# Kernel optimization log

Hardware: AMD Instinct MI355X
Metric: run time of the kernel (lower is better)

The kernel has to match this reference:

```python
import jax, jax.numpy as jnp
import numpy as np

TABLE_SIZE = 256
I16_MIN, I16_MAX = -32768.0, 32767.0
I8_MIN, I8_MAX = -128.0, 127.0
MAX_SOFTMAX_VALUE = 1.0
OUT_SCALE = MAX_SOFTMAX_VALUE * 2.0 / 255.0            # int8 output scale
EXP_OUT_SCALE = 2.0 / 65535.0                          # qint16 exp output scale
RECIP_OUT_SCALE = (1.0 / 0.1) * 2.0 / 65535.0          # qint16 reciprocal output scale
# (xmin, xmax, kind) in ascending x order; 'table' = 256-entry LUT, 'line' = linear fit
EXP_REGIONS = [(-40.0, -20.0, 'line'), (-20.0, -10.0, 'table'), (-10.0, 0.0, 'table'), (0.0, 1.0, 'line')]
RECIP_REGIONS = [(0.001, 0.1, 'line'), (0.1, 250.0, 'table'), (250.0, 500.0, 'table'), (500.0, 700.0, 'line')]


def _quant(y, out_scale, qmin, qmax):
    return jnp.clip(jnp.round(y / out_scale), qmin, qmax)


def _piecewise(x, func, regions, out_scale, qmin, qmax):
    """Piecewise quantized approximation of func: constant / line / 256-entry
    table regions, returning quantized (integer-valued float) outputs."""
    left_c = _quant(func(jnp.float32(regions[0][0])), out_scale, qmin, qmax)
    y = left_c * jnp.ones_like(x)
    for xmin, xmax, kind in regions:
        if kind == 'table':
            xs = jnp.linspace(xmin, xmax, TABLE_SIZE)
            tab = _quant(func(xs), out_scale, qmin, qmax)
            idx = jnp.clip(jnp.round((x - xmin) * ((TABLE_SIZE - 1) / (xmax - xmin))), 0, TABLE_SIZE - 1).astype(jnp.int32)
            y_r = tab[idx]
        else:
            y0 = func(jnp.float32(xmin))
            y1 = func(jnp.float32(xmax))
            y_r = _quant(y0 + (x - xmin) * ((y1 - y0) / (xmax - xmin)), out_scale, qmin, qmax)
        y = jnp.where(x >= xmin, y_r, y)
    right_c = _quant(func(jnp.float32(regions[-1][1])), out_scale, qmin, qmax)
    return jnp.where(x > regions[-1][1], right_c, y)


def setup_inputs() -> dict:
    key = jax.random.key(0)
    k1, _ = jax.random.split(key)
    data = jax.random.randint(k1, (32, 128, 80, 80), -128, 128, dtype=jnp.int32)  # int8 repr, zp=0
    data_scale = jnp.array([0.0625], dtype=jnp.float32)
    return {"data": data, "data_scale": data_scale}


def reference(data, data_scale):
    ds = data_scale[0]
    C = data.shape[1]
    shift = float(np.ceil(np.log2(C)))  # rescale_shift for the exp-sum
    # max-subtract in the integer domain, dequantize diff (zero_point = 0)
    qmax = jnp.max(data, axis=1, keepdims=True)
    xd = (data - qmax).astype(jnp.float32) * ds  # [B,C,H,W], in (-inf, 0]
    # quantized exp via piecewise tables -> qint16 with EXP_OUT_SCALE
    exp_q = _piecewise(xd, jnp.exp, EXP_REGIONS, EXP_OUT_SCALE, I16_MIN, I16_MAX)
    # sum over channels, right-shift back into int16 range
    sum_q = jnp.sum(exp_q, axis=1, keepdims=True)
    sum_sh = jnp.clip(jnp.round(sum_q * (2.0 ** -shift)), I16_MIN, I16_MAX)
    div_scale = EXP_OUT_SCALE * (2.0 ** shift)  # div_data_scale
    # quantized reciprocal of the (dequantized) shifted sum -> qint16
    recip_q = _piecewise(sum_sh * div_scale, lambda v: 1.0 / v, RECIP_REGIONS, RECIP_OUT_SCALE, I16_MIN, I16_MAX)
    # out = exp * recip, requantized to int8 with OUT_SCALE, then dequantized
    out_q = jnp.clip(jnp.round(exp_q * recip_q * (EXP_OUT_SCALE * RECIP_OUT_SCALE / OUT_SCALE)), I8_MIN, I8_MAX)
    return out_q * OUT_SCALE
```

## Files before the change

### kernel.cpp

```cpp
#include <hip/hip_runtime.h>
#include <cmath>

#define NB  32
#define NC  128
#define NHW 6400
#define PIX 64
#define TPB 256

typedef float vfloat4 __attribute__((ext_vector_type(4)));


__global__ __launch_bounds__(TPB) void qsoftmax_kernel(
    const int* __restrict__ data,
    const float* __restrict__ dscale,
    float* __restrict__ out) {
#pragma clang fp contract(off)
  __shared__ int   exp_tab[256];
  __shared__ float recip_tab[256];
  __shared__ int4  red_m[16][16];
  __shared__ int4  red_s[16][16];

  const int t  = threadIdx.x;
  const int k  = t >> 4;
  const int p4 = t & 15;

  const int blk  = blockIdx.x;
  const int b    = blk / (NHW / PIX);
  const int hw0  = (blk % (NHW / PIX)) * PIX;
  const int base4 = b * NC * (NHW / 4) + (hw0 >> 2);

  const float ds = dscale[0];

  {
    const float EXP_SCALE_F = (float)(2.0 / 65535.0);
    float x = (float)(-t) * ds;
    float e;
    if (x >= 0.0f) {
      float y0 = expf(0.0f), y1 = expf(1.0f);
      e = rintf((y0 + x * ((y1 - y0) / 1.0f)) / EXP_SCALE_F);
    } else if (x >= -10.0f) {
      float delta = 10.0f / 255.0f;
      float idxf = rintf((x + 10.0f) * 25.5f);
      idxf = fminf(fmaxf(idxf, 0.0f), 255.0f);
      float xs = -10.0f + idxf * delta;
      e = rintf((float)exp((double)xs) / EXP_SCALE_F);
    } else {
      float delta = 10.0f / 255.0f;
      float idxf = rintf((x + 20.0f) * 25.5f);
      idxf = fminf(fmaxf(idxf, 0.0f), 255.0f);
      float xs = -20.0f + idxf * delta;
      e = rintf((float)exp((double)xs) / EXP_SCALE_F);
    }
    e = fminf(fmaxf(e, -32768.0f), 32767.0f);
    exp_tab[t] = (int)e;

    const float RECIP_SCALE_F = (float)((1.0 / 0.1) * 2.0 / 65535.0);
    float deltar = (250.0f - 0.1f) / 255.0f;
    float xs = 0.1f + (float)t * deltar;
    float r = rintf((1.0f / xs) / RECIP_SCALE_F);
    r = fminf(fmaxf(r, -32768.0f), 32767.0f);
    recip_tab[t] = r;
  }

  const int4* g4 = (const int4*)data;
  int pd[8];
  int4 m = make_int4(-128, -128, -128, -128);
#pragma unroll
  for (int i = 0; i < 8; ++i) {
    int4 v = g4[base4 + (16 * i + k) * (NHW / 4) + p4];
    m.x = max(m.x, v.x); m.y = max(m.y, v.y);
    m.z = max(m.z, v.z); m.w = max(m.w, v.w);
    pd[i] = (v.x & 255) | ((v.y & 255) << 8) | ((v.z & 255) << 16) |
            (int)((unsigned)(v.w & 255) << 24);
  }
  red_m[k][p4] = m;
  __syncthreads();

  int4 q = red_m[0][p4];
#pragma unroll
  for (int kk = 1; kk < 16; ++kk) {
    int4 r = red_m[kk][p4];
    q.x = max(q.x, r.x); q.y = max(q.y, r.y);
    q.z = max(q.z, r.z); q.w = max(q.w, r.w);
  }

  int pe[16];
  int4 s = make_int4(0, 0, 0, 0);
#pragma unroll
  for (int i = 0; i < 8; ++i) {
    int pdv = pd[i];
    int c0 = (pdv << 24) >> 24;
    int c1 = (pdv << 16) >> 24;
    int c2 = (pdv << 8) >> 24;
    int c3 = pdv >> 24;
    int e0 = exp_tab[q.x - c0];
    int e1 = exp_tab[q.y - c1];
    int e2 = exp_tab[q.z - c2];
    int e3 = exp_tab[q.w - c3];
    s.x += e0; s.y += e1; s.z += e2; s.w += e3;
    pe[2 * i]     = e0 | (e1 << 16);
    pe[2 * i + 1] = e2 | (e3 << 16);
  }
  red_s[k][p4] = s;
  __syncthreads();

  int4 tot = red_s[0][p4];
#pragma unroll
  for (int kk = 1; kk < 16; ++kk) {
    int4 r = red_s[kk][p4];
    tot.x += r.x; tot.y += r.y; tot.z += r.z; tot.w += r.w;
  }
  const float DIV_SCALE_F = (float)((2.0 / 65535.0) * 128.0);
  const float RIDX_K_F    = (float)(255.0 / (250.0 - 0.1));
  float rq[4];
  {
    int tv[4] = {tot.x, tot.y, tot.z, tot.w};
#pragma unroll
    for (int j = 0; j < 4; ++j) {
      float ss = rintf((float)tv[j] * 0.0078125f);
      ss = fminf(fmaxf(ss, -32768.0f), 32767.0f);
      float v = ss * DIV_SCALE_F;
      float idxf = rintf((v - 0.1f) * RIDX_K_F);
      idxf = fminf(fmaxf(idxf, 0.0f), 255.0f);
      rq[j] = recip_tab[(int)idxf];
    }
  }

  const float K_F = (float)((2.0 / 65535.0) * ((1.0 / 0.1) * 2.0 / 65535.0) / (2.0 / 255.0));
  const float OUT_SCALE_F = (float)(2.0 / 255.0);
  vfloat4* o4 = (vfloat4*)out;
#pragma unroll
  for (int i = 0; i < 8; ++i) {
    int pa = pe[2 * i], pb = pe[2 * i + 1];
    float e0 = (float)(pa & 0xFFFF);
    float e1 = (float)(pa >> 16);
    float e2 = (float)(pb & 0xFFFF);
    float e3 = (float)(pb >> 16);
    vfloat4 o;
    o.x = fminf(fmaxf(rintf((e0 * rq[0]) * K_F), -128.0f), 127.0f) * OUT_SCALE_F;
    o.y = fminf(fmaxf(rintf((e1 * rq[1]) * K_F), -128.0f), 127.0f) * OUT_SCALE_F;
    o.z = fminf(fmaxf(rintf((e2 * rq[2]) * K_F), -128.0f), 127.0f) * OUT_SCALE_F;
    o.w = fminf(fmaxf(rintf((e3 * rq[3]) * K_F), -128.0f), 127.0f) * OUT_SCALE_F;
    __builtin_nontemporal_store(o, &o4[base4 + (16 * i + k) * (NHW / 4) + p4]);
  }
}

extern "C" void kernel_launch(void* const* d_in, const int* in_sizes, int n_in,
                              void* d_out, int out_size, void* d_ws, size_t ws_size,
                              hipStream_t stream) {
  const int* data     = (const int*)d_in[0];
  const float* dscale = (const float*)d_in[1];
  float* out          = (float*)d_out;
  (void)in_sizes; (void)n_in; (void)d_ws; (void)ws_size; (void)out_size;

  dim3 grid(NB * (NHW / PIX));
  qsoftmax_kernel<<<grid, TPB, 0, stream>>>(data, dscale, out);
}
```

Measured before the change: 187.8 us.

## Assign one pixel per thread over all channels, removing shared-memory reductions

Each thread now handles one spatial position across all 128 channels, so the channel max and exp-sum are done in registers and the two shared-memory reduction passes plus one barrier are gone. Loads and stores become scalar 4-byte accesses, coalesced across threads, in place of int4 vectors. The exp table is stored as floats and indexed with packed byte-wise subtraction, and exp values are re-looked-up in the output pass rather than kept packed. The cost is heavy register use (32 packed words per thread), fewer threads per block, and less memory-level parallelism from the narrower accesses.

```diff
diff --git a/kernel.cpp b/kernel.cpp
--- a/kernel.cpp
+++ b/kernel.cpp
@@ -4,10 +4,8 @@
 #define NB  32
 #define NC  128
 #define NHW 6400
-#define PIX 64
-#define TPB 256
-
-typedef float vfloat4 __attribute__((ext_vector_type(4)));
+#define TPB 128
+#define BPB (NHW / TPB)
 
 
 __global__ __launch_bounds__(TPB) void qsoftmax_kernel(
@@ -15,25 +13,17 @@
     const float* __restrict__ dscale,
     float* __restrict__ out) {
 #pragma clang fp contract(off)
-  __shared__ int   exp_tab[256];
+  __shared__ float exp_tab_f[256];
   __shared__ float recip_tab[256];
-  __shared__ int4  red_m[16][16];
-  __shared__ int4  red_s[16][16];
 
-  const int t  = threadIdx.x;
-  const int k  = t >> 4;
-  const int p4 = t & 15;
-
-  const int blk  = blockIdx.x;
-  const int b    = blk / (NHW / PIX);
-  const int hw0  = (blk % (NHW / PIX)) * PIX;
-  const int base4 = b * NC * (NHW / 4) + (hw0 >> 2);
-
+  const int t = threadIdx.x;
   const float ds = dscale[0];
 
-  {
+#pragma unroll
+  for (int e2 = 0; e2 < 2; ++e2) {
+    const int idx = t + e2 * TPB;
     const float EXP_SCALE_F = (float)(2.0 / 65535.0);
-    float x = (float)(-t) * ds;
+    float x = (float)(-idx) * ds;
     float e;
     if (x >= 0.0f) {
       float y0 = expf(0.0f), y1 = expf(1.0f);
@@ -52,96 +42,84 @@
       e = rintf((float)exp((double)xs) / EXP_SCALE_F);
     }
     e = fminf(fmaxf(e, -32768.0f), 32767.0f);
-    exp_tab[t] = (int)e;
+    exp_tab_f[idx] = e;
 
     const float RECIP_SCALE_F = (float)((1.0 / 0.1) * 2.0 / 65535.0);
     float deltar = (250.0f - 0.1f) / 255.0f;
-    float xs = 0.1f + (float)t * deltar;
+    float xs = 0.1f + (float)idx * deltar;
     float r = rintf((1.0f / xs) / RECIP_SCALE_F);
     r = fminf(fmaxf(r, -32768.0f), 32767.0f);
-    recip_tab[t] = r;
+    recip_tab[idx] = r;
+  }
+  __syncthreads();
+
+  const int b    = blockIdx.x / BPB;
+  const int hw   = (blockIdx.x % BPB) * TPB + t;
+  const int base = b * NC * NHW + hw;
+
+  int pd[32];
+  int q = -128;
+#pragma unroll
+  for (int g = 0; g < 32; ++g) {
+    int v0 = data[base + (4 * g + 0) * NHW];
+    int v1 = data[base + (4 * g + 1) * NHW];
+    int v2 = data[base + (4 * g + 2) * NHW];
+    int v3 = data[base + (4 * g + 3) * NHW];
+    q = max(q, max(max(v0, v1), max(v2, v3)));
+    pd[g] = (v0 & 255) | ((v1 & 255) << 8) | ((v2 & 255) << 16) |
+            (int)((unsigned)(v3 & 255) << 24);
   }
 
-  const int4* g4 = (const int4*)data;
-  int pd[8];
-  int4 m = make_int4(-128, -128, -128, -128);
+  {
+    unsigned qq   = (unsigned)q & 255u;
+    unsigned Qe_g = (((qq << 16) | qq) + 0x01000100u);
+    unsigned Qo_g = Qe_g << 8;
 #pragma unroll
-  for (int i = 0; i < 8; ++i) {
-    int4 v = g4[base4 + (16 * i + k) * (NHW / 4) + p4];
-    m.x = max(m.x, v.x); m.y = max(m.y, v.y);
-    m.z = max(m.z, v.z); m.w = max(m.w, v.w);
-    pd[i] = (v.x & 255) | ((v.y & 255) << 8) | ((v.z & 255) << 16) |
-            (int)((unsigned)(v.w & 255) << 24);
-  }
-  red_m[k][p4] = m;
-  __syncthreads();
-
-  int4 q = red_m[0][p4];
-#pragma unroll
-  for (int kk = 1; kk < 16; ++kk) {
-    int4 r = red_m[kk][p4];
-    q.x = max(q.x, r.x); q.y = max(q.y, r.y);
-    q.z = max(q.z, r.z); q.w = max(q.w, r.w);
-  }
-
-  int pe[16];
-  int4 s = make_int4(0, 0, 0, 0);
-#pragma unroll
-  for (int i = 0; i < 8; ++i) {
-    int pdv = pd[i];
-    int c0 = (pdv << 24) >> 24;
-    int c1 = (pdv << 16) >> 24;
-    int c2 = (pdv << 8) >> 24;
-    int c3 = pdv >> 24;
-    int e0 = exp_tab[q.x - c0];
-    int e1 = exp_tab[q.y - c1];
-    int e2 = exp_tab[q.z - c2];
-    int e3 = exp_tab[q.w - c3];
-    s.x += e0; s.y += e1; s.z += e2; s.w += e3;
-    pe[2 * i]     = e0 | (e1 << 16);
-    pe[2 * i + 1] = e2 | (e3 << 16);
-  }
-  red_s[k][p4] = s;
-  __syncthreads();
-
-  int4 tot = red_s[0][p4];
-#pragma unroll
-  for (int kk = 1; kk < 16; ++kk) {
-    int4 r = red_s[kk][p4];
-    tot.x += r.x; tot.y += r.y; tot.z += r.z; tot.w += r.w;
-  }
-  const float DIV_SCALE_F = (float)((2.0 / 65535.0) * 128.0);
-  const float RIDX_K_F    = (float)(255.0 / (250.0 - 0.1));
-  float rq[4];
-  {
-    int tv[4] = {tot.x, tot.y, tot.z, tot.w};
-#pragma unroll
-    for (int j = 0; j < 4; ++j) {
-      float ss = rintf((float)tv[j] * 0.0078125f);
-      ss = fminf(fmaxf(ss, -32768.0f), 32767.0f);
-      float v = ss * DIV_SCALE_F;
-      float idxf = rintf((v - 0.1f) * RIDX_K_F);
-      idxf = fminf(fmaxf(idxf, 0.0f), 255.0f);
-      rq[j] = recip_tab[(int)idxf];
+    for (int g = 0; g < 32; ++g) {
+      unsigned p  = (unsigned)pd[g];
+      unsigned je = (Qe_g - (p & 0x00FF00FFu)) & 0x00FF00FFu;
+      unsigned jo = (Qo_g - (p & 0xFF00FF00u)) & 0xFF00FF00u;
+      pd[g] = (int)(je | jo);
     }
   }
 
+  float s0 = 0.f, s1 = 0.f, s2 = 0.f, s3 = 0.f;
+#pragma unroll
+  for (int g = 0; g < 32; ++g) {
+    unsigned J = (unsigned)pd[g];
+    s0 += exp_tab_f[J & 255u];
+    s1 += exp_tab_f[(J >> 8) & 255u];
+    s2 += exp_tab_f[(J >> 16) & 255u];
+    s3 += exp_tab_f[J >> 24];
+  }
+  float tot = (s0 + s1) + (s2 + s3);
+
+  const float DIV_SCALE_F = (float)((2.0 / 65535.0) * 128.0);
+  const float RIDX_K_F    = (float)(255.0 / (250.0 - 0.1));
+  float ss = rintf(tot * 0.0078125f);
+  ss = fminf(fmaxf(ss, -32768.0f), 32767.0f);
+  float v = ss * DIV_SCALE_F;
+  float idxf = rintf((v - 0.1f) * RIDX_K_F);
+  idxf = fminf(fmaxf(idxf, 0.0f), 255.0f);
+  const float rq = recip_tab[(int)idxf];
+
   const float K_F = (float)((2.0 / 65535.0) * ((1.0 / 0.1) * 2.0 / 65535.0) / (2.0 / 255.0));
   const float OUT_SCALE_F = (float)(2.0 / 255.0);
-  vfloat4* o4 = (vfloat4*)out;
 #pragma unroll
-  for (int i = 0; i < 8; ++i) {
-    int pa = pe[2 * i], pb = pe[2 * i + 1];
-    float e0 = (float)(pa & 0xFFFF);
-    float e1 = (float)(pa >> 16);
-    float e2 = (float)(pb & 0xFFFF);
-    float e3 = (float)(pb >> 16);
-    vfloat4 o;
-    o.x = fminf(fmaxf(rintf((e0 * rq[0]) * K_F), -128.0f), 127.0f) * OUT_SCALE_F;
-    o.y = fminf(fmaxf(rintf((e1 * rq[1]) * K_F), -128.0f), 127.0f) * OUT_SCALE_F;
-    o.z = fminf(fmaxf(rintf((e2 * rq[2]) * K_F), -128.0f), 127.0f) * OUT_SCALE_F;
-    o.w = fminf(fmaxf(rintf((e3 * rq[3]) * K_F), -128.0f), 127.0f) * OUT_SCALE_F;
-    __builtin_nontemporal_store(o, &o4[base4 + (16 * i + k) * (NHW / 4) + p4]);
+  for (int g = 0; g < 32; ++g) {
+    unsigned J = (unsigned)pd[g];
+    float e0 = exp_tab_f[J & 255u];
+    float e1 = exp_tab_f[(J >> 8) & 255u];
+    float e2 = exp_tab_f[(J >> 16) & 255u];
+    float e3 = exp_tab_f[J >> 24];
+    float o0 = fminf(fmaxf(rintf((e0 * rq) * K_F), -128.0f), 127.0f) * OUT_SCALE_F;
+    float o1 = fminf(fmaxf(rintf((e1 * rq) * K_F), -128.0f), 127.0f) * OUT_SCALE_F;
+    float o2 = fminf(fmaxf(rintf((e2 * rq) * K_F), -128.0f), 127.0f) * OUT_SCALE_F;
+    float o3 = fminf(fmaxf(rintf((e3 * rq) * K_F), -128.0f), 127.0f) * OUT_SCALE_F;
+    __builtin_nontemporal_store(o0, &out[base + (4 * g + 0) * NHW]);
+    __builtin_nontemporal_store(o1, &out[base + (4 * g + 1) * NHW]);
+    __builtin_nontemporal_store(o2, &out[base + (4 * g + 2) * NHW]);
+    __builtin_nontemporal_store(o3, &out[base + (4 * g + 3) * NHW]);
   }
 }
 
@@ -153,6 +131,6 @@
   float* out          = (float*)d_out;
   (void)in_sizes; (void)n_in; (void)d_ws; (void)ws_size; (void)out_size;
 
-  dim3 grid(NB * (NHW / PIX));
+  dim3 grid(NB * BPB);
   qsoftmax_kernel<<<grid, TPB, 0, stream>>>(data, dscale, out);
 }
```

Result: slower. 207.5 us (+10.5%).

## Enlarge blocks to 1024 threads and pack SIMD byte-wise index diffs

Applied to the files above, without the earlier changes.

Each block now uses 1024 threads over 256 pixels instead of 256 threads over 64 pixels. This gives longer contiguous row segments per channel and amortizes the per-block LUT build over more work. The max-minus-value indices are computed with packed SIMD-within-a-register byte arithmetic. The exp table is stored as float and looked up again at output time instead of keeping packed int16 exp values, which lowers register pressure but doubles LDS lookups. Float summation of integer-valued exps stays exact within the range here.

```diff
diff --git a/kernel.cpp b/kernel.cpp
--- a/kernel.cpp
+++ b/kernel.cpp
@@ -1,11 +1,12 @@
 #include <hip/hip_runtime.h>
 #include <cmath>
 
-#define NB  32
-#define NC  128
-#define NHW 6400
-#define PIX 64
-#define TPB 256
+#define NB   32
+#define NC   128
+#define NHW  6400
+#define TPB  1024
+#define PIXB 256
+#define GPB  (NHW / PIXB)
 
 typedef float vfloat4 __attribute__((ext_vector_type(4)));
 
@@ -15,23 +16,18 @@
     const float* __restrict__ dscale,
     float* __restrict__ out) {
 #pragma clang fp contract(off)
-  __shared__ int   exp_tab[256];
+  __shared__ float exp_tab_f[256];
   __shared__ float recip_tab[256];
-  __shared__ int4  red_m[16][16];
-  __shared__ int4  red_s[16][16];
+  __shared__ int4  red_m[16][64];
+  __shared__ float4 red_s[16][64];
 
-  const int t  = threadIdx.x;
-  const int k  = t >> 4;
-  const int p4 = t & 15;
-
-  const int blk  = blockIdx.x;
-  const int b    = blk / (NHW / PIX);
-  const int hw0  = (blk % (NHW / PIX)) * PIX;
-  const int base4 = b * NC * (NHW / 4) + (hw0 >> 2);
+  const int t = threadIdx.x;
+  const int k = t >> 6;
+  const int p = t & 63;
 
   const float ds = dscale[0];
 
-  {
+  if (t < 256) {
     const float EXP_SCALE_F = (float)(2.0 / 65535.0);
     float x = (float)(-t) * ds;
     float e;
@@ -52,7 +48,7 @@
       e = rintf((float)exp((double)xs) / EXP_SCALE_F);
     }
     e = fminf(fmaxf(e, -32768.0f), 32767.0f);
-    exp_tab[t] = (int)e;
+    exp_tab_f[t] = e;
 
     const float RECIP_SCALE_F = (float)((1.0 / 0.1) * 2.0 / 65535.0);
     float deltar = (250.0f - 0.1f) / 255.0f;
@@ -62,62 +58,70 @@
     recip_tab[t] = r;
   }
 
-  const int4* g4 = (const int4*)data;
+  const int blk   = blockIdx.x;
+  const int b     = blk / GPB;
+  const int base4 = b * NC * (NHW / 4) + (blk % GPB) * (PIXB / 4) + p;
+  const int4* g4  = (const int4*)data;
+
   int pd[8];
   int4 m = make_int4(-128, -128, -128, -128);
 #pragma unroll
   for (int i = 0; i < 8; ++i) {
-    int4 v = g4[base4 + (16 * i + k) * (NHW / 4) + p4];
+    int4 v = g4[base4 + (16 * i + k) * (NHW / 4)];
     m.x = max(m.x, v.x); m.y = max(m.y, v.y);
     m.z = max(m.z, v.z); m.w = max(m.w, v.w);
     pd[i] = (v.x & 255) | ((v.y & 255) << 8) | ((v.z & 255) << 16) |
             (int)((unsigned)(v.w & 255) << 24);
   }
-  red_m[k][p4] = m;
+  red_m[k][p] = m;
   __syncthreads();
 
-  int4 q = red_m[0][p4];
+  int4 q = red_m[0][p];
 #pragma unroll
   for (int kk = 1; kk < 16; ++kk) {
-    int4 r = red_m[kk][p4];
+    int4 r = red_m[kk][p];
     q.x = max(q.x, r.x); q.y = max(q.y, r.y);
     q.z = max(q.z, r.z); q.w = max(q.w, r.w);
   }
 
-  int pe[16];
-  int4 s = make_int4(0, 0, 0, 0);
+  {
+    unsigned Qe = (((unsigned)q.x & 255u) | (((unsigned)q.z & 255u) << 16)) + 0x01000100u;
+    unsigned Qo = ((((unsigned)q.y & 255u) << 8) | (((unsigned)q.w & 255u) << 24)) + 0x00010000u;
+#pragma unroll
+    for (int i = 0; i < 8; ++i) {
+      unsigned pp = (unsigned)pd[i];
+      unsigned je = (Qe - (pp & 0x00FF00FFu)) & 0x00FF00FFu;
+      unsigned jo = (Qo - (pp & 0xFF00FF00u)) & 0xFF00FF00u;
+      pd[i] = (int)(je | jo);
+    }
+  }
+
+  float sx = 0.f, sy = 0.f, sz = 0.f, sw = 0.f;
 #pragma unroll
   for (int i = 0; i < 8; ++i) {
-    int pdv = pd[i];
-    int c0 = (pdv << 24) >> 24;
-    int c1 = (pdv << 16) >> 24;
-    int c2 = (pdv << 8) >> 24;
-    int c3 = pdv >> 24;
-    int e0 = exp_tab[q.x - c0];
-    int e1 = exp_tab[q.y - c1];
-    int e2 = exp_tab[q.z - c2];
-    int e3 = exp_tab[q.w - c3];
-    s.x += e0; s.y += e1; s.z += e2; s.w += e3;
-    pe[2 * i]     = e0 | (e1 << 16);
-    pe[2 * i + 1] = e2 | (e3 << 16);
+    unsigned J = (unsigned)pd[i];
+    sx += exp_tab_f[J & 255u];
+    sy += exp_tab_f[(J >> 8) & 255u];
+    sz += exp_tab_f[(J >> 16) & 255u];
+    sw += exp_tab_f[J >> 24];
   }
-  red_s[k][p4] = s;
+  red_s[k][p] = make_float4(sx, sy, sz, sw);
   __syncthreads();
 
-  int4 tot = red_s[0][p4];
+  float4 tot = red_s[0][p];
 #pragma unroll
   for (int kk = 1; kk < 16; ++kk) {
-    int4 r = red_s[kk][p4];
+    float4 r = red_s[kk][p];
     tot.x += r.x; tot.y += r.y; tot.z += r.z; tot.w += r.w;
   }
   const float DIV_SCALE_F = (float)((2.0 / 65535.0) * 128.0);
   const float RIDX_K_F    = (float)(255.0 / (250.0 - 0.1));
   float rq[4];
   {
-    int tv[4] = {tot.x, tot.y, tot.z, tot.w};
+    float tv[4] = {tot.x, tot.y, tot.z, tot.w};
 #pragma unroll
     for (int j = 0; j < 4; ++j) {
-      float ss = rintf((float)tv[j] * 0.0078125f);
+      float ss = rintf(tv[j] * 0.0078125f);
       ss = fminf(fmaxf(ss, -32768.0f), 32767.0f);
       float v = ss * DIV_SCALE_F;
       float idxf = rintf((v - 0.1f) * RIDX_K_F);
@@ -131,17 +135,17 @@
   vfloat4* o4 = (vfloat4*)out;
 #pragma unroll
   for (int i = 0; i < 8; ++i) {
-    int pa = pe[2 * i], pb = pe[2 * i + 1];
-    float e0 = (float)(pa & 0xFFFF);
-    float e1 = (float)(pa >> 16);
-    float e2 = (float)(pb & 0xFFFF);
-    float e3 = (float)(pb >> 16);
+    unsigned J = (unsigned)pd[i];
+    float e0 = exp_tab_f[J & 255u];
+    float e1 = exp_tab_f[(J >> 8) & 255u];
+    float e2 = exp_tab_f[(J >> 16) & 255u];
+    float e3 = exp_tab_f[J >> 24];
     vfloat4 o;
     o.x = fminf(fmaxf(rintf((e0 * rq[0]) * K_F), -128.0f), 127.0f) * OUT_SCALE_F;
     o.y = fminf(fmaxf(rintf((e1 * rq[1]) * K_F), -128.0f), 127.0f) * OUT_SCALE_F;
     o.z = fminf(fmaxf(rintf((e2 * rq[2]) * K_F), -128.0f), 127.0f) * OUT_SCALE_F;
     o.w = fminf(fmaxf(rintf((e3 * rq[3]) * K_F), -128.0f), 127.0f) * OUT_SCALE_F;
-    __builtin_nontemporal_store(o, &o4[base4 + (16 * i + k) * (NHW / 4) + p4]);
+    __builtin_nontemporal_store(o, &o4[base4 + (16 * i + k) * (NHW / 4)]);
   }
 }
 
@@ -153,6 +157,6 @@
   float* out          = (float*)d_out;
   (void)in_sizes; (void)n_in; (void)d_ws; (void)ws_size; (void)out_size;
 
-  dim3 grid(NB * (NHW / PIX));
+  dim3 grid(NB * GPB);
   qsoftmax_kernel<<<grid, TPB, 0, stream>>>(data, dscale, out);
 }
```

After: 194.1 us. 3.4% more time.

## Replace shared-memory channel reductions with DPP row shuffles and packed byte indexing

Applied to the files above, without the earlier changes.

Remaps threads so the 16 lanes of a DPP row hold the channel groups of one pixel quad. Max and sum reductions then use cross-lane DPP moves instead of shared-memory arrays and barriers. Table indices are computed with packed byte arithmetic, and the exp table is stored as float. The remap shortens the contiguous global segment each wavefront load touches, which may hurt memory coalescing.

```diff
diff --git a/kernel.cpp b/kernel.cpp
--- a/kernel.cpp
+++ b/kernel.cpp
@@ -6,28 +6,46 @@
 #define NHW 6400
 #define PIX 64
 #define TPB 256
+#define BPB (NHW / PIX)
 
 typedef float vfloat4 __attribute__((ext_vector_type(4)));
 
+
+template <int CTRL>
+__device__ __forceinline__ int dpp_mov(int x) {
+  return __builtin_amdgcn_update_dpp(x, x, CTRL, 0xF, 0xF, true);
+}
+#define DPP_XOR1 0xB1
+#define DPP_XOR2 0x4E
+#define DPP_ROR4 0x124
+#define DPP_ROR8 0x128
+
+template <int CTRL>
+__device__ __forceinline__ void dpp_max4(int4& m) {
+  m.x = max(m.x, dpp_mov<CTRL>(m.x));
+  m.y = max(m.y, dpp_mov<CTRL>(m.y));
+  m.z = max(m.z, dpp_mov<CTRL>(m.z));
+  m.w = max(m.w, dpp_mov<CTRL>(m.w));
+}
+template <int CTRL>
+__device__ __forceinline__ void dpp_add4(int4& s) {
+  s.x += dpp_mov<CTRL>(s.x);
+  s.y += dpp_mov<CTRL>(s.y);
+  s.z += dpp_mov<CTRL>(s.z);
+  s.w += dpp_mov<CTRL>(s.w);
+}
 
 __global__ __launch_bounds__(TPB) void qsoftmax_kernel(
     const int* __restrict__ data,
     const float* __restrict__ dscale,
     float* __restrict__ out) {
 #pragma clang fp contract(off)
-  __shared__ int   exp_tab[256];
+  __shared__ float exp_tab_f[256];
   __shared__ float recip_tab[256];
-  __shared__ int4  red_m[16][16];
-  __shared__ int4  red_s[16][16];
 
-  const int t  = threadIdx.x;
-  const int k  = t >> 4;
-  const int p4 = t & 15;
-
-  const int blk  = blockIdx.x;
-  const int b    = blk / (NHW / PIX);
-  const int hw0  = (blk % (NHW / PIX)) * PIX;
-  const int base4 = b * NC * (NHW / 4) + (hw0 >> 2);
+  const int t = threadIdx.x;
+  const int k = t & 15;
+  const int q = t >> 4;
 
   const float ds = dscale[0];
 
@@ -52,7 +70,7 @@
       e = rintf((float)exp((double)xs) / EXP_SCALE_F);
     }
     e = fminf(fmaxf(e, -32768.0f), 32767.0f);
-    exp_tab[t] = (int)e;
+    exp_tab_f[t] = e;
 
     const float RECIP_SCALE_F = (float)((1.0 / 0.1) * 2.0 / 65535.0);
     float deltar = (250.0f - 0.1f) / 255.0f;
@@ -61,60 +79,65 @@
     r = fminf(fmaxf(r, -32768.0f), 32767.0f);
     recip_tab[t] = r;
   }
+  __syncthreads();
 
-  const int4* g4 = (const int4*)data;
+  const int blk   = blockIdx.x;
+  const int b     = blk / BPB;
+  const int base4 = b * NC * (NHW / 4) + (blk % BPB) * (PIX / 4) + q;
+  const int4* g4  = (const int4*)data;
+
   int pd[8];
   int4 m = make_int4(-128, -128, -128, -128);
 #pragma unroll
   for (int i = 0; i < 8; ++i) {
-    int4 v = g4[base4 + (16 * i + k) * (NHW / 4) + p4];
+    int4 v = g4[base4 + (16 * i + k) * (NHW / 4)];
     m.x = max(m.x, v.x); m.y = max(m.y, v.y);
     m.z = max(m.z, v.z); m.w = max(m.w, v.w);
     pd[i] = (v.x & 255) | ((v.y & 255) << 8) | ((v.z & 255) << 16) |
             (int)((unsigned)(v.w & 255) << 24);
   }
-  red_m[k][p4] = m;
-  __syncthreads();
 
-  int4 q = red_m[0][p4];
+  dpp_max4<DPP_XOR1>(m);
+  dpp_max4<DPP_XOR2>(m);
+  dpp_max4<DPP_ROR4>(m);
+  dpp_max4<DPP_ROR8>(m);
+
+  {
+    unsigned Qe = (((unsigned)m.x & 255u) | (((unsigned)m.z & 255u) << 16)) + 0x01000100u;
+    unsigned Qo = ((((unsigned)m.y & 255u) << 8) | (((unsigned)m.w & 255u) << 24)) + 0x00010000u;
 #pragma unroll
-  for (int kk = 1; kk < 16; ++kk) {
-    int4 r = red_m[kk][p4];
-    q.x = max(q.x, r.x); q.y = max(q.y, r.y);
-    q.z = max(q.z, r.z); q.w = max(q.w, r.w);
+    for (int i = 0; i < 8; ++i) {
+      unsigned pp = (unsigned)pd[i];
+      unsigned je = (Qe - (pp & 0x00FF00FFu)) & 0x00FF00FFu;
+      unsigned jo = (Qo - (pp & 0xFF00FF00u)) & 0xFF00FF00u;
+      pd[i] = (int)(je | jo);
+    }
   }
 
   int pe[16];
   int4 s = make_int4(0, 0, 0, 0);
 #pragma unroll
   for (int i = 0; i < 8; ++i) {
-    int pdv = pd[i];
-    int c0 = (pdv << 24) >> 24;
-    int c1 = (pdv << 16) >> 24;
-    int c2 = (pdv << 8) >> 24;
-    int c3 = pdv >> 24;
-    int e0 = exp_tab[q.x - c0];
-    int e1 = exp_tab[q.y - c1];
-    int e2 = exp_tab[q.z - c2];
-    int e3 = exp_tab[q.w - c3];
+    unsigned J = (unsigned)pd[i];
+    int e0 = (int)exp_tab_f[J & 255u];
+    int e1 = (int)exp_tab_f[(J >> 8) & 255u];
+    int e2 = (int)exp_tab_f[(J >> 16) & 255u];
+    int e3 = (int)exp_tab_f[J >> 24];
     s.x += e0; s.y += e1; s.z += e2; s.w += e3;
     pe[2 * i]     = e0 | (e1 << 16);
     pe[2 * i + 1] = e2 | (e3 << 16);
   }
-  red_s[k][p4] = s;
-  __syncthreads();
 
-  int4 tot = red_s[0][p4];
-#pragma unroll
-  for (int kk = 1; kk < 16; ++kk) {
-    int4 r = red_s[kk][p4];
-    tot.x += r.x; tot.y += r.y; tot.z += r.z; tot.w += r.w;
-  }
+  dpp_add4<DPP_XOR1>(s);
+  dpp_add4<DPP_XOR2>(s);
+  dpp_add4<DPP_ROR4>(s);
+  dpp_add4<DPP_ROR8>(s);
+
   const float DIV_SCALE_F = (float)((2.0 / 65535.0) * 128.0);
   const float RIDX_K_F    = (float)(255.0 / (250.0 - 0.1));
   float rq[4];
   {
-    int tv[4] = {tot.x, tot.y, tot.z, tot.w};
+    int tv[4] = {s.x, s.y, s.z, s.w};
 #pragma unroll
     for (int j = 0; j < 4; ++j) {
       float ss = rintf((float)tv[j] * 0.0078125f);
@@ -141,7 +164,7 @@
     o.y = fminf(fmaxf(rintf((e1 * rq[1]) * K_F), -128.0f), 127.0f) * OUT_SCALE_F;
     o.z = fminf(fmaxf(rintf((e2 * rq[2]) * K_F), -128.0f), 127.0f) * OUT_SCALE_F;
     o.w = fminf(fmaxf(rintf((e3 * rq[3]) * K_F), -128.0f), 127.0f) * OUT_SCALE_F;
-    __builtin_nontemporal_store(o, &o4[base4 + (16 * i + k) * (NHW / 4) + p4]);
+    __builtin_nontemporal_store(o, (vfloat4*)&o4[base4 + (16 * i + k) * (NHW / 4)]);
   }
 }
 
@@ -153,6 +176,6 @@
   float* out          = (float*)d_out;
   (void)in_sizes; (void)n_in; (void)d_ws; (void)ws_size; (void)out_size;
 
-  dim3 grid(NB * (NHW / PIX));
+  dim3 grid(NB * BPB);
   qsoftmax_kernel<<<grid, TPB, 0, stream>>>(data, dscale, out);
 }
```

New measurement: 202.7 us. 1.08x slower.
